# Optimization experiments

Measured on AMD Instinct MI355X. Metric: run time of the kernel, lower is better.

The kernel has to match this reference:

```python
import jax, jax.numpy as jnp
import numpy as np
from jax import lax

B, C, T = 16, 32, 512
GAF_SIZE = 128
LATENT = 128
EPS = 1e-8


def _conv(x, w, b, stride):
    # x: (N, Cin, H, W), w: (Cout, Cin, kh, kw)
    y = lax.conv_general_dilated(x, w, (stride, stride), 'SAME',
                                 dimension_numbers=('NCHW', 'OIHW', 'NCHW'))
    return jax.nn.relu(y + b[None, :, None, None])


def _compute_gaf(x_raw):
    # x_raw: (B, C, T) -> (B*C, 2, S, S) with channels [GASF, GADF]
    S = GAF_SIZE
    # Piecewise Aggregate Approximation: T -> S
    x = x_raw.reshape(B, C, S, T // S).mean(axis=-1)        # (B, C, S)
    # Min-max normalize each series to [-1, 1]
    mn = x.min(axis=-1, keepdims=True)
    mx = x.max(axis=-1, keepdims=True)
    x = jnp.clip(2.0 * (x - mn) / (mx - mn + EPS) - 1.0, -1.0, 1.0)
    # phi = arccos(x); use trig identities to avoid explicit arccos
    sq = jnp.sqrt(jnp.clip(1.0 - x * x, 0.0, 1.0))          # sin(phi)
    xi, xj = x[..., :, None], x[..., None, :]
    si, sj = sq[..., :, None], sq[..., None, :]
    gasf = xi * xj - si * sj                                 # cos(phi_i + phi_j)
    gadf = si * xj - xi * sj                                 # sin(phi_i - phi_j)
    gaf = jnp.stack([gasf, gadf], axis=2)                    # (B, C, 2, S, S)
    return gaf.reshape(B * C, 2, S, S).astype(jnp.float32)


def _encoder(gaf, W1, b1, W2, b2, W3, b3, W4, b4, Wfc, bfc):
    h = _conv(gaf, W1, b1, 2)   # (B*C, 32, 64, 64)
    h = _conv(h, W2, b2, 2)     # (B*C, 64, 32, 32)
    h = _conv(h, W3, b3, 2)     # (B*C, 128, 16, 16)
    h = _conv(h, W4, b4, 2)     # (B*C, 256, 8, 8)
    h = h.mean(axis=(2, 3))     # global average pool -> (B*C, 256)
    return h @ Wfc + bfc        # (B*C, LATENT)


def setup_inputs() -> dict:
    key = jax.random.key(0)
    ks = jax.random.split(key, 12)
    p = lambda k, shp: (jax.random.normal(k, shp, dtype=jnp.float32) * 0.05)
    return {
        'x_raw': jax.random.normal(ks[0], (B, C, T), dtype=jnp.float32),
        'W1': p(ks[1], (32, 2, 3, 3)),   'b1': jnp.zeros((32,), jnp.float32),
        'W2': p(ks[2], (64, 32, 3, 3)),  'b2': jnp.zeros((64,), jnp.float32),
        'W3': p(ks[3], (128, 64, 3, 3)), 'b3': jnp.zeros((128,), jnp.float32),
        'W4': p(ks[4], (256, 128, 3, 3)),'b4': jnp.zeros((256,), jnp.float32),
        'Wfc': p(ks[5], (256, LATENT)),  'bfc': jnp.zeros((LATENT,), jnp.float32),
    }


def reference(x_raw, W1, b1, W2, b2, W3, b3, W4, b4, Wfc, bfc):
    # GAF computed from detached raw EEG in the original (numpy CPU path)
    gaf = lax.stop_gradient(_compute_gaf(x_raw))
    z = _encoder(gaf, W1, b1, W2, b2, W3, b3, W4, b4, Wfc, bfc)
    return z.reshape(B, C, LATENT).mean(axis=1)              # (B, LATENT)
```

## Files before the change

### kernel.cpp

```cpp
#include <hip/hip_runtime.h>
#include <hip/hip_bf16.h>

#define DEV __device__ __forceinline__

constexpr int kB = 16, kC = 32, kT = 512, kS = 128, kBC = 512, kLatent = 128;
constexpr float kEps = 1e-8f;

using bf16 = __hip_bfloat16;
using bf16x8 = __attribute__((ext_vector_type(8))) short;
using f32x4  = __attribute__((ext_vector_type(4))) float;

DEV unsigned short f2bf(float v) {
    bf16 h = __float2bfloat16(v);
    return *(unsigned short*)&h;
}

DEV void gld16(const void* g, void* l) {
    __builtin_amdgcn_global_load_lds(
        (const __attribute__((address_space(1))) unsigned*)g,
        (__attribute__((address_space(3))) unsigned*)l, 16, 0, 0);
}

__global__ void gaf_stats_kernel(const float* __restrict__ x_raw,
                                 float* __restrict__ xn, float* __restrict__ sq) {
    int bc = blockIdx.x;
    int s  = threadIdx.x;
    const float* xp = x_raw + (size_t)bc * kT;
    float v = 0.25f * (xp[4*s] + xp[4*s+1] + xp[4*s+2] + xp[4*s+3]);
    __shared__ float smn[kS], smx[kS];
    smn[s] = v; smx[s] = v;
    __syncthreads();
    for (int off = kS/2; off > 0; off >>= 1) {
        if (s < off) {
            smn[s] = fminf(smn[s], smn[s+off]);
            smx[s] = fmaxf(smx[s], smx[s+off]);
        }
        __syncthreads();
    }
    float mn = smn[0], mx = smx[0];
    float xv = 2.0f * (v - mn) / (mx - mn + kEps) - 1.0f;
    xv = fminf(fmaxf(xv, -1.0f), 1.0f);
    float sv = sqrtf(fminf(fmaxf(1.0f - xv*xv, 0.0f), 1.0f));
    xn[bc*kS + s] = xv;
    sq[bc*kS + s] = sv;
}

__global__ void wtrans_all_kernel(const float* __restrict__ w1,
                                  const float* __restrict__ w2,
                                  const float* __restrict__ w3,
                                  const float* __restrict__ w4,
                                  bf16* __restrict__ w1b, bf16* __restrict__ wt2,
                                  bf16* __restrict__ wt3, bf16* __restrict__ wt4) {
    int idx = blockIdx.x * blockDim.x + threadIdx.x;
    if (idx < 1024) {
        int oc = idx >> 5, k = idx & 31;
        w1b[idx] = __float2bfloat16(k < 18 ? w1[oc*18 + k] : 0.0f);
        return;
    }
    idx -= 1024;
    const float* src; bf16* dst; int CIN, COUT;
    if (idx < 18432)       { src = w2; dst = wt2; CIN = 32;  COUT = 64;  }
    else if (idx < 92160)  { idx -= 18432;  src = w3; dst = wt3; CIN = 64;  COUT = 128; }
    else if (idx < 387072) { idx -= 92160;  src = w4; dst = wt4; CIN = 128; COUT = 256; }
    else return;
    int ic = idx % CIN;
    int oc = (idx / CIN) % COUT;
    int t  = idx / (CIN * COUT);
    dst[((size_t)t * COUT + oc) * CIN + ic] = __float2bfloat16(src[((size_t)oc * CIN + ic) * 9 + t]);
}

__global__ __launch_bounds__(256, 2)
void conv12_kernel(const float* __restrict__ xn, const float* __restrict__ sq,
                   const bf16* __restrict__ w1b, const float* __restrict__ b1,
                   const bf16* __restrict__ wt2, const float* __restrict__ b2,
                   bf16* __restrict__ out, int img0) {
    __shared__ float xl[kS], sl[kS];
    __shared__ __align__(16) union { short G[576][40]; short H[2][288][40]; } U;
    __shared__ __align__(16) short Bs2[3][64][32];
    __shared__ __align__(16) short W1s[32][40];

    int tid  = threadIdx.x;
    int lane = tid & 63;
    int wv   = tid >> 6;
    int mblk = blockIdx.x;
    int bz   = blockIdx.y;
    int bc   = img0 + bz;

    gld16((const char*)wt2 + 0*4096 + tid*16, (char*)Bs2 + 0*4096 + tid*16);
    gld16((const char*)wt2 + 1*4096 + tid*16, (char*)Bs2 + 1*4096 + tid*16);

    if (tid < 128) {
        xl[tid] = xn[(size_t)bc * kS + tid];
        int rr = tid >> 2, sg = tid & 3;
        *(uint4*)&W1s[rr][sg*8] = *(const uint4*)(w1b + rr*32 + sg*8);
    } else {
        sl[tid - 128] = sq[(size_t)bc * kS + (tid - 128)];
    }
    __syncthreads();

    #pragma unroll
    for (int it = 0; it < 3; ++it) {
        int idx = it * 256 + tid;
        if (idx >= 576) break;
        int trow = idx >> 6, hx = idx & 63;
        int iy = 8 * mblk + trow;
        unsigned int pk[16];
        #pragma unroll
        for (int j = 0; j < 16; ++j) pk[j] = 0u;
        if (iy < 64) {
            float xr[3], sr[3], xc[3], sc[3];
            #pragma unroll
            for (int k = 0; k < 3; ++k) {
                int iyy = 2*iy + k, ixx = 2*hx + k;
                bool vy = iyy < kS, vx = ixx < kS;
                xr[k] = vy ? xl[iyy] : 0.0f;  sr[k] = vy ? sl[iyy] : 0.0f;
                xc[k] = vx ? xl[ixx] : 0.0f;  sc[k] = vx ? sl[ixx] : 0.0f;
            }
            unsigned short gs[18];
            #pragma unroll
            for (int ky = 0; ky < 3; ++ky)
                #pragma unroll
                for (int kx = 0; kx < 3; ++kx) {
                    gs[ky*3+kx]   = f2bf(xr[ky]*xc[kx] - sr[ky]*sc[kx]);
                    gs[9+ky*3+kx] = f2bf(sr[ky]*xc[kx] - xr[ky]*sc[kx]);
                }
            #pragma unroll
            for (int j = 0; j < 9; ++j)
                pk[j] = (unsigned int)gs[2*j] | ((unsigned int)gs[2*j+1] << 16);
        }
        #pragma unroll
        for (int j = 0; j < 4; ++j) *(uint4*)&U.G[idx][j*8] = ((uint4*)pk)[j];
    }
    __syncthreads();

    f32x4 c1[9][2];
    bf16x8 w1f0 = *(const bf16x8*)&W1s[(lane & 15)][(lane>>4)*8];
    bf16x8 w1f1 = *(const bf16x8*)&W1s[16 + (lane & 15)][(lane>>4)*8];
    #pragma unroll
    for (int j = 0; j < 9; ++j) {
        int mt = 4*j + wv;
        bf16x8 af = *(const bf16x8*)&U.G[mt*16 + (lane & 15)][(lane>>4)*8];
        f32x4 zz = f32x4{0.f, 0.f, 0.f, 0.f};
        c1[j][0] = __builtin_amdgcn_mfma_f32_16x16x32_bf16(af, w1f0, zz, 0, 0, 0);
        c1[j][1] = __builtin_amdgcn_mfma_f32_16x16x32_bf16(af, w1f1, zz, 0, 0, 0);
    }
    __syncthreads();

    #pragma unroll
    for (int j = 0; j < 9; ++j) {
        int mt = 4*j + wv;
        #pragma unroll
        for (int h = 0; h < 2; ++h) {
            int oc = h*16 + (lane & 15);
            float bb = b1[oc];
            #pragma unroll
            for (int rg = 0; rg < 4; ++rg) {
                int pos = mt*16 + (lane>>4)*4 + rg;
                int trow = pos >> 6, hx = pos & 63;
                float v = fmaxf(c1[j][h][rg] + bb, 0.0f);
                if (8*mblk + trow >= 64) v = 0.0f;
                U.H[hx & 1][trow*32 + (hx >> 1)][oc] = (short)f2bf(v);
            }
        }
    }
    __syncthreads();

    f32x4 acc[2][4];
    #pragma unroll
    for (int i = 0; i < 2; ++i)
        #pragma unroll
        for (int j = 0; j < 4; ++j) acc[i][j] = f32x4{0.f, 0.f, 0.f, 0.f};

    for (int tap = 0; tap < 9; ++tap) {
        if (tap + 2 < 9)
            gld16((const char*)wt2 + (tap+2)*4096 + tid*16,
                  (char*)Bs2 + ((tap+2)%3)*4096 + tid*16);
        int ky = tap / 3, kx = tap % 3;
        int trow = 2*wv + ky;
        const short* bsl = &Bs2[tap%3][0][0];
        bf16x8 af[2], bfr[4];
        #pragma unroll
        for (int mi = 0; mi < 2; ++mi) {
            int ocol = mi*16 + (lane & 15);
            int x = 2*ocol + kx;
            bf16x8 z = {0,0,0,0,0,0,0,0};
            af[mi] = (x < 64) ? *(const bf16x8*)&U.H[kx & 1][trow*32 + (x>>1)][(lane>>4)*8] : z;
        }
        #pragma unroll
        for (int ni = 0; ni < 4; ++ni)
            bfr[ni] = *(const bf16x8*)&bsl[(ni*16 + (lane&15))*32 + (lane>>4)*8];
        #pragma unroll
        for (int mi = 0; mi < 2; ++mi)
            #pragma unroll
            for (int ni = 0; ni < 4; ++ni)
                acc[mi][ni] = __builtin_amdgcn_mfma_f32_16x16x32_bf16(af[mi], bfr[ni], acc[mi][ni], 0, 0, 0);
        __syncthreads();
    }

    int oy = 4*mblk + wv;
    #pragma unroll
    for (int ni = 0; ni < 4; ++ni) {
        int oc = ni*16 + (lane & 15);
        float b = b2[oc];
        #pragma unroll
        for (int mi = 0; mi < 2; ++mi)
            #pragma unroll
            for (int rg = 0; rg < 4; ++rg) {
                int ocol = 16*mi + (lane>>4)*4 + rg;
                float v = fmaxf(acc[mi][ni][rg] + b, 0.0f);
                out[(((size_t)bz*32 + oy)*32 + ocol)*64 + oc] = __float2bfloat16(v);
            }
    }
}

template<int CIN, int COUT, int HIN, int IMGS, bool POOL>
__global__ __launch_bounds__(256, 4)
void conv_mfma_kernel(const bf16* __restrict__ in, const bf16* __restrict__ wt,
                      const float* __restrict__ bias, bf16* __restrict__ out,
                      float* __restrict__ pooled, int img0,
                      const bf16* __restrict__ zbuf) {
    constexpr int HOUT = HIN / 2;
    constexpr int PPI  = HOUT * HOUT;
    constexpr int K    = 9 * CIN;
    constexpr int S    = K / 32;
    constexpr int TPC  = CIN / 32;
    __shared__ __align__(16) short As[2*128*32];
    __shared__ __align__(16) short Bs[2*128*32];

    int tid  = threadIdx.x;
    int lane = tid & 63;
    int wv   = tid >> 6;
    int wm   = wv >> 1, wn = wv & 1;
    int bx   = blockIdx.x;
    int nblk = blockIdx.y;
    int bz   = blockIdx.z;

    int rsub = lane >> 2, seg = lane & 3;
    int imgA[2], oyA[2], oxA[2], rB[2];
    #pragma unroll
    for (int j = 0; j < 2; ++j) {
        int r = (wv*2 + j)*16 + rsub;
        int il, pos;
        if (IMGS > 1) { il = bz*IMGS + r/PPI; pos = r % PPI; }
        else          { il = bz; pos = bx*128 + r; }
        imgA[j] = il; oyA[j] = pos / HOUT; oxA[j] = pos % HOUT;
        rB[j] = r;
    }

    auto issue = [&](int s, int nb) {
        int tap = s / TPC, icb = (s % TPC) * 32;
        int ky = tap / 3, kx = tap % 3;
        #pragma unroll
        for (int j = 0; j < 2; ++j) {
            int iy = 2*oyA[j] + ky, ix = 2*oxA[j] + kx;
            const bf16* ga = (iy < HIN && ix < HIN)
                ? in + (((size_t)imgA[j]*HIN + iy)*HIN + ix)*CIN + icb + seg*8
                : zbuf + seg*8;
            gld16(ga, (char*)As + nb*8192 + (wv*2 + j)*1024 + lane*16);
            const bf16* gb = wt + ((size_t)tap*COUT + nblk*128 + rB[j])*CIN + icb + seg*8;
            gld16(gb, (char*)Bs + nb*8192 + (wv*2 + j)*1024 + lane*16);
        }
    };

    f32x4 acc[4][4];
    #pragma unroll
    for (int i = 0; i < 4; ++i)
        #pragma unroll
        for (int j = 0; j < 4; ++j) acc[i][j] = f32x4{0.f, 0.f, 0.f, 0.f};

    issue(0, 0);
    __syncthreads();

    for (int s = 0; s < S; ++s) {
        int cur = s & 1;
        if (s + 1 < S) issue(s + 1, cur ^ 1);
        bf16x8 af[4], bfr[4];
        #pragma unroll
        for (int mi = 0; mi < 4; ++mi)
            af[mi] = *(const bf16x8*)&As[cur*4096 + (wm*64 + mi*16 + (lane&15))*32 + (lane>>4)*8];
        #pragma unroll
        for (int ni = 0; ni < 4; ++ni)
            bfr[ni] = *(const bf16x8*)&Bs[cur*4096 + (wn*64 + ni*16 + (lane&15))*32 + (lane>>4)*8];
        #pragma unroll
        for (int mi = 0; mi < 4; ++mi)
            #pragma unroll
            for (int ni = 0; ni < 4; ++ni)
                acc[mi][ni] = __builtin_amdgcn_mfma_f32_16x16x32_bf16(af[mi], bfr[ni], acc[mi][ni], 0, 0, 0);
        __syncthreads();
    }

    if (!POOL) {
        #pragma unroll
        for (int ni = 0; ni < 4; ++ni) {
            int oc = nblk*128 + wn*64 + ni*16 + (lane & 15);
            float b = bias[oc];
            #pragma unroll
            for (int mi = 0; mi < 4; ++mi)
                #pragma unroll
                for (int rg = 0; rg < 4; ++rg) {
                    int rr = wm*64 + mi*16 + (lane>>4)*4 + rg;
                    int img_e, pos_e;
                    if (IMGS > 1) { img_e = bz*IMGS + rr/PPI; pos_e = rr % PPI; }
                    else          { img_e = bz; pos_e = bx*128 + rr; }
                    int oye = pos_e / HOUT, oxe = pos_e % HOUT;
                    float v = fmaxf(acc[mi][ni][rg] + b, 0.0f);
                    out[(((size_t)img_e * HOUT + oye) * HOUT + oxe) * COUT + oc] = __float2bfloat16(v);
                }
        }
    } else {
        int img_e = bz*IMGS + wm;
        #pragma unroll
        for (int ni = 0; ni < 4; ++ni) {
            int oc = nblk*128 + wn*64 + ni*16 + (lane & 15);
            float b = bias[oc];
            float s = 0.0f;
            #pragma unroll
            for (int mi = 0; mi < 4; ++mi)
                #pragma unroll
                for (int rg = 0; rg < 4; ++rg) s += fmaxf(acc[mi][ni][rg] + b, 0.0f);
            s += __shfl_xor(s, 16);
            s += __shfl_xor(s, 32);
            if (lane < 16)
                pooled[((size_t)(img0 + img_e))*256 + nblk*128 + wn*64 + ni*16 + lane] = s * (1.0f/64.0f);
        }
    }
}

__global__ void poolfc_kernel(const float* __restrict__ pooled, const float* __restrict__ Wfc,
                              const float* __restrict__ bfc, float* __restrict__ out) {
    int b = blockIdx.x;
    int t = threadIdx.x;
    __shared__ float pm[256];
    #pragma unroll
    for (int q = 0; q < 2; ++q) {
        int k = q*128 + t;
        float s = 0.0f;
        #pragma unroll
        for (int c = 0; c < kC; ++c) s += pooled[((size_t)(b*kC + c))*256 + k];
        pm[k] = s * (1.0f/kC);
    }
    __syncthreads();
    float acc = bfc[t];
    for (int k = 0; k < 256; ++k) acc = fmaf(pm[k], Wfc[(size_t)k*kLatent + t], acc);
    out[(size_t)b*kLatent + t] = acc;
}

extern "C" void kernel_launch(void* const* d_in, const int* in_sizes, int n_in,
                              void* d_out, int out_size, void* d_ws, size_t ws_size,
                              hipStream_t stream) {
    const float* x_raw = (const float*)d_in[0];
    const float* W1 = (const float*)d_in[1];  const float* b1 = (const float*)d_in[2];
    const float* W2 = (const float*)d_in[3];  const float* b2 = (const float*)d_in[4];
    const float* W3 = (const float*)d_in[5];  const float* b3 = (const float*)d_in[6];
    const float* W4 = (const float*)d_in[7];  const float* b4 = (const float*)d_in[8];
    const float* Wfc = (const float*)d_in[9]; const float* bfc = (const float*)d_in[10];
    float* out = (float*)d_out;

    char* wsb = (char*)d_ws;
    float* xn     = (float*)(wsb);
    float* sq     = (float*)(wsb + (256u<<10));
    float* pooled = (float*)(wsb + (512u<<10));
    bf16* Wt2     = (bf16*)(wsb + (1280u<<10));
    bf16* Wt3     = (bf16*)(wsb + (1316u<<10));
    bf16* Wt4     = (bf16*)(wsb + (1460u<<10));
    bf16* W1b     = (bf16*)(wsb + (2036u<<10));
    bf16* zbuf    = (bf16*)(wsb + (2040u<<10));
    char* chunk_base = wsb + (2048u<<10);

    const size_t perH2 = 32u*32u*64u*2u, perH3 = 16u*16u*128u*2u;
    const size_t perImg = perH2 + perH3;
    int chunk = 4;
    for (int c = 512; c >= 4; c >>= 1) {
        if ((2048u<<10) + (size_t)c * perImg <= ws_size) { chunk = c; break; }
    }

    hipMemsetAsync(zbuf, 0, 1024, stream);
    gaf_stats_kernel<<<kBC, kS, 0, stream>>>(x_raw, xn, sq);
    wtrans_all_kernel<<<(388096 + 255)/256, 256, 0, stream>>>(W1, W2, W3, W4, W1b, Wt2, Wt3, Wt4);

    for (int img0 = 0; img0 < kBC; img0 += chunk) {
        int nimg = chunk;
        bf16* h2 = (bf16*)chunk_base;
        bf16* h3 = (bf16*)(chunk_base + (size_t)chunk * perH2);

        conv12_kernel<<<dim3(8, nimg), 256, 0, stream>>>(xn, sq, W1b, b1, Wt2, b2, h2, img0);
        conv_mfma_kernel<64, 128, 32, 1, false>
            <<<dim3(2, 1, nimg), 256, 0, stream>>>(h2, Wt3, b3, h3, nullptr, img0, zbuf);
        conv_mfma_kernel<128, 256, 16, 2, true>
            <<<dim3(1, 2, nimg/2), 256, 0, stream>>>(h3, Wt4, b4, nullptr, pooled, img0, zbuf);
    }

    poolfc_kernel<<<kB, kLatent, 0, stream>>>(pooled, Wfc, bfc, out);
}
```

Measured before the change: 255.4 us.

## Fuse conv3 and conv4 into one per-image kernel keeping h3 in LDS

Replaces the two templated implicit-GEMM conv kernels for layers 3 and 4 with a single kernel that handles one image per block. Conv3 output stays in shared memory with an XOR swizzle, and conv4 reads its A operand straight from LDS with im2col indexing, followed by fused ReLU and average pooling. This removes the global write and re-read of h3 plus one launch per chunk. In exchange, LDS use rises to roughly 130KB per block, which limits occupancy to about one block per CU, and only 512 blocks cover the whole grid.

```diff
diff --git a/kernel.cpp b/kernel.cpp
--- a/kernel.cpp
+++ b/kernel.cpp
@@ -213,116 +213,140 @@
     }
 }
 
-template<int CIN, int COUT, int HIN, int IMGS, bool POOL>
-__global__ __launch_bounds__(256, 4)
-void conv_mfma_kernel(const bf16* __restrict__ in, const bf16* __restrict__ wt,
-                      const float* __restrict__ bias, bf16* __restrict__ out,
-                      float* __restrict__ pooled, int img0,
-                      const bf16* __restrict__ zbuf) {
-    constexpr int HOUT = HIN / 2;
-    constexpr int PPI  = HOUT * HOUT;
-    constexpr int K    = 9 * CIN;
-    constexpr int S    = K / 32;
-    constexpr int TPC  = CIN / 32;
-    __shared__ __align__(16) short As[2*128*32];
-    __shared__ __align__(16) short Bs[2*128*32];
+__global__ __launch_bounds__(256)
+void conv34_kernel(const bf16* __restrict__ h2, const bf16* __restrict__ wt3,
+                   const float* __restrict__ b3, const bf16* __restrict__ wt4,
+                   const float* __restrict__ b4, float* __restrict__ pooled,
+                   int img0, const bf16* __restrict__ zbuf) {
+    __shared__ __align__(16) short H3[257*128];
+    __shared__ __align__(16) short stA[2*256*32];
+    __shared__ __align__(16) short stB[2*128*32];
 
     int tid  = threadIdx.x;
     int lane = tid & 63;
     int wv   = tid >> 6;
-    int wm   = wv >> 1, wn = wv & 1;
-    int bx   = blockIdx.x;
-    int nblk = blockIdx.y;
-    int bz   = blockIdx.z;
-
-    int rsub = lane >> 2, seg = lane & 3;
-    int imgA[2], oyA[2], oxA[2], rB[2];
-    #pragma unroll
-    for (int j = 0; j < 2; ++j) {
-        int r = (wv*2 + j)*16 + rsub;
-        int il, pos;
-        if (IMGS > 1) { il = bz*IMGS + r/PPI; pos = r % PPI; }
-        else          { il = bz; pos = bx*128 + r; }
-        imgA[j] = il; oyA[j] = pos / HOUT; oxA[j] = pos % HOUT;
-        rB[j] = r;
-    }
-
-    auto issue = [&](int s, int nb) {
-        int tap = s / TPC, icb = (s % TPC) * 32;
+    int img  = blockIdx.x;
+
+    if (tid < 128) H3[256*128 + tid] = 0;
+
+    auto issue1 = [&](int s, int buf) {
+        int tap = s >> 1, icb = (s & 1) * 32;
         int ky = tap / 3, kx = tap % 3;
         #pragma unroll
+        for (int j = 0; j < 4; ++j) {
+            int row = wv*64 + j*16 + (lane >> 2);
+            int oy = row >> 4, ox = row & 15;
+            int iy = 2*oy + ky, ix = 2*ox + kx;
+            const bf16* src = (iy < 32 && ix < 32)
+                ? h2 + (((size_t)img*32 + iy)*32 + ix)*64 + icb + (lane & 3)*8
+                : zbuf + (lane & 3)*8;
+            gld16(src, (char*)&stA[buf*8192 + (wv*64 + j*16)*32] + lane*16);
+        }
+        #pragma unroll
         for (int j = 0; j < 2; ++j) {
-            int iy = 2*oyA[j] + ky, ix = 2*oxA[j] + kx;
-            const bf16* ga = (iy < HIN && ix < HIN)
-                ? in + (((size_t)imgA[j]*HIN + iy)*HIN + ix)*CIN + icb + seg*8
-                : zbuf + seg*8;
-            gld16(ga, (char*)As + nb*8192 + (wv*2 + j)*1024 + lane*16);
-            const bf16* gb = wt + ((size_t)tap*COUT + nblk*128 + rB[j])*CIN + icb + seg*8;
-            gld16(gb, (char*)Bs + nb*8192 + (wv*2 + j)*1024 + lane*16);
+            int brow = wv*32 + j*16 + (lane >> 2);
+            const bf16* src = wt3 + ((size_t)tap*128 + brow)*64 + icb + (lane & 3)*8;
+            gld16(src, (char*)&stB[buf*4096 + (wv*32 + j*16)*32] + lane*16);
         }
     };
 
-    f32x4 acc[4][4];
+    f32x4 acc[4][8];
     #pragma unroll
     for (int i = 0; i < 4; ++i)
         #pragma unroll
-        for (int j = 0; j < 4; ++j) acc[i][j] = f32x4{0.f, 0.f, 0.f, 0.f};
-
-    issue(0, 0);
-    __syncthreads();
-
-    for (int s = 0; s < S; ++s) {
+        for (int j = 0; j < 8; ++j) acc[i][j] = f32x4{0.f, 0.f, 0.f, 0.f};
+
+    issue1(0, 0);
+    __syncthreads();
+
+    for (int s = 0; s < 18; ++s) {
         int cur = s & 1;
-        if (s + 1 < S) issue(s + 1, cur ^ 1);
-        bf16x8 af[4], bfr[4];
+        if (s + 1 < 18) issue1(s + 1, cur ^ 1);
+        bf16x8 af[4];
         #pragma unroll
         for (int mi = 0; mi < 4; ++mi)
-            af[mi] = *(const bf16x8*)&As[cur*4096 + (wm*64 + mi*16 + (lane&15))*32 + (lane>>4)*8];
-        #pragma unroll
-        for (int ni = 0; ni < 4; ++ni)
-            bfr[ni] = *(const bf16x8*)&Bs[cur*4096 + (wn*64 + ni*16 + (lane&15))*32 + (lane>>4)*8];
+            af[mi] = *(const bf16x8*)&stA[cur*8192 + (wv*64 + mi*16 + (lane&15))*32 + (lane>>4)*8];
+        #pragma unroll
+        for (int ni = 0; ni < 8; ++ni) {
+            bf16x8 bfr = *(const bf16x8*)&stB[cur*4096 + (ni*16 + (lane&15))*32 + (lane>>4)*8];
+            #pragma unroll
+            for (int mi = 0; mi < 4; ++mi)
+                acc[mi][ni] = __builtin_amdgcn_mfma_f32_16x16x32_bf16(af[mi], bfr, acc[mi][ni], 0, 0, 0);
+        }
+        __syncthreads();
+    }
+
+    #pragma unroll
+    for (int ni = 0; ni < 8; ++ni) {
+        int oc = ni*16 + (lane & 15);
+        float bb = b3[oc];
+        int q = oc >> 3, ql = oc & 7;
         #pragma unroll
         for (int mi = 0; mi < 4; ++mi)
             #pragma unroll
-            for (int ni = 0; ni < 4; ++ni)
-                acc[mi][ni] = __builtin_amdgcn_mfma_f32_16x16x32_bf16(af[mi], bfr[ni], acc[mi][ni], 0, 0, 0);
+            for (int rg = 0; rg < 4; ++rg) {
+                int pos = wv*64 + mi*16 + (lane>>4)*4 + rg;
+                float v = fmaxf(acc[mi][ni][rg] + bb, 0.0f);
+                H3[pos*128 + (q ^ ((pos>>1)&7))*8 + ql] = (short)f2bf(v);
+            }
+    }
+
+    auto issue2 = [&](int s, int buf) {
+        int tap = s >> 2, icb = (s & 3) * 32;
+        #pragma unroll
+        for (int j = 0; j < 4; ++j) {
+            int brow = wv*64 + j*16 + (lane >> 2);
+            const bf16* src = wt4 + ((size_t)tap*256 + brow)*128 + icb + (lane & 3)*8;
+            gld16(src, (char*)&stA[buf*8192 + (wv*64 + j*16)*32] + lane*16);
+        }
+    };
+
+    issue2(0, 0);
+    __syncthreads();
+
+    f32x4 ac4[4][4];
+    #pragma unroll
+    for (int i = 0; i < 4; ++i)
+        #pragma unroll
+        for (int j = 0; j < 4; ++j) ac4[i][j] = f32x4{0.f, 0.f, 0.f, 0.f};
+
+    for (int s = 0; s < 36; ++s) {
+        int cur = s & 1;
+        if (s + 1 < 36) issue2(s + 1, cur ^ 1);
+        int tap = s >> 2, kq0 = (s & 3) * 4 + (lane >> 4);
+        int ky = tap / 3, kx = tap % 3;
+        bf16x8 af[4];
+        #pragma unroll
+        for (int mi = 0; mi < 4; ++mi) {
+            int m = mi*16 + (lane & 15);
+            int oy = m >> 3, ox = m & 7;
+            int iy = 2*oy + ky, ix = 2*ox + kx;
+            int pos = (iy < 16 && ix < 16) ? iy*16 + ix : 256;
+            af[mi] = *(const bf16x8*)&H3[pos*128 + (kq0 ^ ((pos>>1)&7))*8];
+        }
+        #pragma unroll
+        for (int ni = 0; ni < 4; ++ni) {
+            bf16x8 bfr = *(const bf16x8*)&stA[cur*8192 + (wv*64 + ni*16 + (lane&15))*32 + (lane>>4)*8];
+            #pragma unroll
+            for (int mi = 0; mi < 4; ++mi)
+                ac4[mi][ni] = __builtin_amdgcn_mfma_f32_16x16x32_bf16(af[mi], bfr, ac4[mi][ni], 0, 0, 0);
+        }
         __syncthreads();
     }
 
-    if (!POOL) {
-        #pragma unroll
-        for (int ni = 0; ni < 4; ++ni) {
-            int oc = nblk*128 + wn*64 + ni*16 + (lane & 15);
-            float b = bias[oc];
-            #pragma unroll
-            for (int mi = 0; mi < 4; ++mi)
-                #pragma unroll
-                for (int rg = 0; rg < 4; ++rg) {
-                    int rr = wm*64 + mi*16 + (lane>>4)*4 + rg;
-                    int img_e, pos_e;
-                    if (IMGS > 1) { img_e = bz*IMGS + rr/PPI; pos_e = rr % PPI; }
-                    else          { img_e = bz; pos_e = bx*128 + rr; }
-                    int oye = pos_e / HOUT, oxe = pos_e % HOUT;
-                    float v = fmaxf(acc[mi][ni][rg] + b, 0.0f);
-                    out[(((size_t)img_e * HOUT + oye) * HOUT + oxe) * COUT + oc] = __float2bfloat16(v);
-                }
-        }
-    } else {
-        int img_e = bz*IMGS + wm;
-        #pragma unroll
-        for (int ni = 0; ni < 4; ++ni) {
-            int oc = nblk*128 + wn*64 + ni*16 + (lane & 15);
-            float b = bias[oc];
-            float s = 0.0f;
-            #pragma unroll
-            for (int mi = 0; mi < 4; ++mi)
-                #pragma unroll
-                for (int rg = 0; rg < 4; ++rg) s += fmaxf(acc[mi][ni][rg] + b, 0.0f);
-            s += __shfl_xor(s, 16);
-            s += __shfl_xor(s, 32);
-            if (lane < 16)
-                pooled[((size_t)(img0 + img_e))*256 + nblk*128 + wn*64 + ni*16 + lane] = s * (1.0f/64.0f);
-        }
+    #pragma unroll
+    for (int ni = 0; ni < 4; ++ni) {
+        int oc = wv*64 + ni*16 + (lane & 15);
+        float bb = b4[oc];
+        float ssum = 0.0f;
+        #pragma unroll
+        for (int mi = 0; mi < 4; ++mi)
+            #pragma unroll
+            for (int rg = 0; rg < 4; ++rg) ssum += fmaxf(ac4[mi][ni][rg] + bb, 0.0f);
+        ssum += __shfl_xor(ssum, 16);
+        ssum += __shfl_xor(ssum, 32);
+        if (lane < 16)
+            pooled[((size_t)(img0 + img))*256 + wv*64 + ni*16 + lane] = ssum * (1.0f/64.0f);
     }
 }
 
@@ -367,8 +391,7 @@
     bf16* zbuf    = (bf16*)(wsb + (2040u<<10));
     char* chunk_base = wsb + (2048u<<10);
 
-    const size_t perH2 = 32u*32u*64u*2u, perH3 = 16u*16u*128u*2u;
-    const size_t perImg = perH2 + perH3;
+    const size_t perImg = 32u*32u*64u*2u;
     int chunk = 4;
     for (int c = 512; c >= 4; c >>= 1) {
         if ((2048u<<10) + (size_t)c * perImg <= ws_size) { chunk = c; break; }
@@ -381,13 +404,9 @@
     for (int img0 = 0; img0 < kBC; img0 += chunk) {
         int nimg = chunk;
         bf16* h2 = (bf16*)chunk_base;
-        bf16* h3 = (bf16*)(chunk_base + (size_t)chunk * perH2);
 
         conv12_kernel<<<dim3(8, nimg), 256, 0, stream>>>(xn, sq, W1b, b1, Wt2, b2, h2, img0);
-        conv_mfma_kernel<64, 128, 32, 1, false>
-            <<<dim3(2, 1, nimg), 256, 0, stream>>>(h2, Wt3, b3, h3, nullptr, img0, zbuf);
-        conv_mfma_kernel<128, 256, 16, 2, true>
-            <<<dim3(1, 2, nimg/2), 256, 0, stream>>>(h3, Wt4, b4, nullptr, pooled, img0, zbuf);
+        conv34_kernel<<<nimg, 256, 0, stream>>>(h2, Wt3, b3, Wt4, b4, pooled, img0, zbuf);
     }
 
     poolfc_kernel<<<kB, kLatent, 0, stream>>>(pooled, Wfc, bfc, out);
```

After: 244.4 us. 4.3% less time.

## Load conv2 weights into registers directly and reorder conv K loop to tap-inner

Applied to the files above, without the earlier changes.

In the fused conv1+conv2 kernel, conv2 weight fragments are now read straight from global memory into registers with one-tap prefetch. This replaces the triple-buffered LDS staging, which removes the shared buffer and the per-tap __syncthreads and raises the occupancy hint from 2 to 3 blocks per CU. Separately, the generic conv kernel now walks its K dimension with taps innermost and channel blocks outermost, which changes the global access order of the input and weight loads. The register prefetch adds register pressure, and every wave now fetches weights from global or cache instead of sharing one LDS copy.

```diff
diff --git a/kernel.cpp b/kernel.cpp
--- a/kernel.cpp
+++ b/kernel.cpp
@@ -69,14 +69,13 @@
     dst[((size_t)t * COUT + oc) * CIN + ic] = __float2bfloat16(src[((size_t)oc * CIN + ic) * 9 + t]);
 }
 
-__global__ __launch_bounds__(256, 2)
+__global__ __launch_bounds__(256, 3)
 void conv12_kernel(const float* __restrict__ xn, const float* __restrict__ sq,
                    const bf16* __restrict__ w1b, const float* __restrict__ b1,
                    const bf16* __restrict__ wt2, const float* __restrict__ b2,
                    bf16* __restrict__ out, int img0) {
     __shared__ float xl[kS], sl[kS];
     __shared__ __align__(16) union { short G[576][40]; short H[2][288][40]; } U;
-    __shared__ __align__(16) short Bs2[3][64][32];
     __shared__ __align__(16) short W1s[32][40];
 
     int tid  = threadIdx.x;
@@ -85,9 +84,6 @@
     int mblk = blockIdx.x;
     int bz   = blockIdx.y;
     int bc   = img0 + bz;
-
-    gld16((const char*)wt2 + 0*4096 + tid*16, (char*)Bs2 + 0*4096 + tid*16);
-    gld16((const char*)wt2 + 1*4096 + tid*16, (char*)Bs2 + 1*4096 + tid*16);
 
     if (tid < 128) {
         xl[tid] = xn[(size_t)bc * kS + tid];
@@ -165,20 +161,26 @@
     }
     __syncthreads();
 
+    auto loadB2 = [&](int tap, bf16x8* dst) {
+        #pragma unroll
+        for (int ni = 0; ni < 4; ++ni) {
+            int row = ni*16 + (lane & 15);
+            dst[ni] = *(const bf16x8*)(wt2 + ((size_t)tap*64 + row)*32 + (lane>>4)*8);
+        }
+    };
     f32x4 acc[2][4];
     #pragma unroll
     for (int i = 0; i < 2; ++i)
         #pragma unroll
         for (int j = 0; j < 4; ++j) acc[i][j] = f32x4{0.f, 0.f, 0.f, 0.f};
 
+    bf16x8 bcur[4], bnxt[4];
+    loadB2(0, bcur);
     for (int tap = 0; tap < 9; ++tap) {
-        if (tap + 2 < 9)
-            gld16((const char*)wt2 + (tap+2)*4096 + tid*16,
-                  (char*)Bs2 + ((tap+2)%3)*4096 + tid*16);
+        if (tap + 1 < 9) loadB2(tap + 1, bnxt);
         int ky = tap / 3, kx = tap % 3;
         int trow = 2*wv + ky;
-        const short* bsl = &Bs2[tap%3][0][0];
-        bf16x8 af[2], bfr[4];
+        bf16x8 af[2];
         #pragma unroll
         for (int mi = 0; mi < 2; ++mi) {
             int ocol = mi*16 + (lane & 15);
@@ -187,14 +189,12 @@
             af[mi] = (x < 64) ? *(const bf16x8*)&U.H[kx & 1][trow*32 + (x>>1)][(lane>>4)*8] : z;
         }
         #pragma unroll
-        for (int ni = 0; ni < 4; ++ni)
-            bfr[ni] = *(const bf16x8*)&bsl[(ni*16 + (lane&15))*32 + (lane>>4)*8];
-        #pragma unroll
         for (int mi = 0; mi < 2; ++mi)
             #pragma unroll
             for (int ni = 0; ni < 4; ++ni)
-                acc[mi][ni] = __builtin_amdgcn_mfma_f32_16x16x32_bf16(af[mi], bfr[ni], acc[mi][ni], 0, 0, 0);
-        __syncthreads();
+                acc[mi][ni] = __builtin_amdgcn_mfma_f32_16x16x32_bf16(af[mi], bcur[ni], acc[mi][ni], 0, 0, 0);
+        #pragma unroll
+        for (int ni = 0; ni < 4; ++ni) bcur[ni] = bnxt[ni];
     }
 
     int oy = 4*mblk + wv;
@@ -221,9 +221,7 @@
                       const bf16* __restrict__ zbuf) {
     constexpr int HOUT = HIN / 2;
     constexpr int PPI  = HOUT * HOUT;
-    constexpr int K    = 9 * CIN;
-    constexpr int S    = K / 32;
-    constexpr int TPC  = CIN / 32;
+    constexpr int S    = 9 * (CIN / 32);
     __shared__ __align__(16) short As[2*128*32];
     __shared__ __align__(16) short Bs[2*128*32];
 
@@ -248,7 +246,8 @@
     }
 
     auto issue = [&](int s, int nb) {
-        int tap = s / TPC, icb = (s % TPC) * 32;
+        int icb = (s / 9) * 32;
+        int tap = s % 9;
         int ky = tap / 3, kx = tap % 3;
         #pragma unroll
         for (int j = 0; j < 2; ++j) {
```

Result: faster. 218.4 us (-14.5%).
